# Performance work log

Hardware: AMD Instinct MI355X
Metric: run time of the kernel (lower is better)

## Reference

```python
import jax, jax.numpy as jnp
import numpy as np

B, T, D = 32, 4096, 256
LN_EPS = 1e-5


def setup_inputs() -> dict:
    key = jax.random.key(0)
    k0, k1, k2 = jax.random.split(key, 3)
    byte_ids = jax.random.randint(k0, (B, T), 0, 256, dtype=jnp.int32)
    freq_bands = jnp.ones((D // 2,), jnp.float32)  # nn.Parameter(torch.ones(embed_dim//2))
    # freq_proj: Linear(D, 2D) -> LayerNorm(2D) -> GELU -> Linear(2D, D)
    w1 = jax.random.normal(k1, (D, 2 * D), jnp.float32) * (1.0 / np.sqrt(D))
    b1 = jnp.zeros((2 * D,), jnp.float32)
    gamma = jnp.ones((2 * D,), jnp.float32)
    beta = jnp.zeros((2 * D,), jnp.float32)
    w2 = jax.random.normal(k2, (2 * D, D), jnp.float32) * (1.0 / np.sqrt(2 * D))
    b2 = jnp.zeros((D,), jnp.float32)
    return dict(byte_ids=byte_ids, freq_bands=freq_bands, w1=w1, b1=b1,
                gamma=gamma, beta=beta, w2=w2, b2=b2)


def reference(byte_ids, freq_bands, w1, b1, gamma, beta, w2, b2):
    Bsz, Tlen = byte_ids.shape
    Dm = w1.shape[0]
    k = min(Dm // 2, Tlen // 2)  # static
    signal = byte_ids.astype(jnp.float32) / 127.5 - 1.0  # [B,T]
    # Single FFT; FFT(roll(signal, -pos))[f] == X[f] * exp(+2i*pi*f*pos/T),
    # so |spectrum| is position-invariant and angle shifts linearly in pos.
    X = jnp.fft.fft(signal, axis=1)[:, :k]           # [B,k] complex64
    mag = jnp.abs(X) * freq_bands[:k]                 # [B,k]
    phase0 = jnp.angle(X)                             # [B,k]
    pos = jnp.arange(Tlen, dtype=jnp.float32)
    f = jnp.arange(k, dtype=jnp.float32)
    shift = (2.0 * np.pi / Tlen) * pos[:, None] * f[None, :]      # [T,k]
    phase = phase0[:, None, :] + shift[None, :, :]                 # [B,T,k]
    mag_bt = jnp.broadcast_to(mag[:, None, :], (Bsz, Tlen, k))     # [B,T,k]
    feats = jnp.concatenate([mag_bt, jnp.sin(phase), jnp.cos(phase)], axis=-1)  # [B,T,3k]
    if feats.shape[-1] < Dm:
        feats = jnp.pad(feats, ((0, 0), (0, 0), (0, Dm - feats.shape[-1])))
    else:
        feats = feats[..., :Dm]                        # truncate (drops cos tail)
    # freq_proj MLP
    h = feats @ w1 + b1                                # [B,T,2D]
    mu = jnp.mean(h, axis=-1, keepdims=True)
    var = jnp.var(h, axis=-1, keepdims=True)
    h = (h - mu) * jax.lax.rsqrt(var + LN_EPS) * gamma + beta
    h = jax.nn.gelu(h, approximate=False)              # torch nn.GELU default = exact erf
    return h @ w2 + b2                                 # [B,T,D]
```

## Files before the change

kernel.cpp:

```cpp
#include <hip/hip_runtime.h>


#define T_SZ   4096
#define NFREQ  128

typedef short    bf16x8 __attribute__((ext_vector_type(8)));
typedef unsigned u32x4  __attribute__((ext_vector_type(4)));
typedef float    f32x4  __attribute__((ext_vector_type(4)));

__device__ __forceinline__ float bf2f(unsigned short x) {
  union { unsigned u; float f; } v; v.u = ((unsigned)x) << 16; return v.f;
}
__device__ __forceinline__ float bits2f(unsigned u) {
  union { unsigned u; float f; } v; v.u = u; return v.f;
}
__device__ __forceinline__ unsigned short f2bf(float x) {
  union { float f; unsigned u; } v; v.f = x;
  unsigned r = v.u + 0x7fffu + ((v.u >> 16) & 1u);
  return (unsigned short)(r >> 16);
}
__device__ __forceinline__ unsigned pk2(float lo, float hi) {
  union { float f; unsigned u; } a, b;
  a.f = lo; b.f = hi;
  return __builtin_amdgcn_perm(b.u + 0x8000u, a.u + 0x8000u, 0x07060302u);
}
__device__ __forceinline__ bf16x8 as_bf(u32x4 v) { return __builtin_bit_cast(bf16x8, v); }
__device__ __forceinline__ bool probe_f32(const unsigned* p) {
  return p[0] == 0x3F800000u;
}
__device__ __forceinline__ void stage16(const void* g, const void* lds_base) {
  __builtin_amdgcn_global_load_lds(
      (const __attribute__((address_space(1))) unsigned int*)g,
      (__attribute__((address_space(3))) unsigned int*)lds_base, 16, 0, 0);
}
__device__ __forceinline__ float gelu_f(float v) {
  float u = v * (0.7978845608f + 0.0356774081f * v * v);
  float d = 1.0f + exp2f(-2.885390082f * u);
  return v * __builtin_amdgcn_rcpf(d);
}

__global__ void dft_kernel(const int* __restrict__ ids,
                           const void* __restrict__ fb,
                           unsigned short* __restrict__ mag,
                           float* __restrict__ ph0) {
  bool f32 = probe_f32((const unsigned*)fb);
  int b  = blockIdx.x >> 3;
  int fg = blockIdx.x & 7;
  int fl = threadIdx.x >> 4;
  int m  = threadIdx.x & 15;
  int f  = fg * 16 + fl;
  const int* row = ids + b * T_SZ;
  const float C = 6.283185307179586f / 4096.0f;
  float re = 0.f, im = 0.f;
  for (int i = 0; i < 256; ++i) {
    int t = m + i * 16;
    float s = (float)row[t] * (1.0f / 127.5f) - 1.0f;
    float ang = (float)((t * f) & 4095) * C;
    re += s * __cosf(ang);
    im -= s * __sinf(ang);
  }
  #pragma unroll
  for (int mask = 1; mask < 16; mask <<= 1) {
    re += __shfl_xor(re, mask, 64);
    im += __shfl_xor(im, mask, 64);
  }
  if (m == 0) {
    float fbv = f32 ? ((const float*)fb)[f] : bf2f(((const unsigned short*)fb)[f]);
    float mg = sqrtf(re * re + im * im) * fbv;
    mag[b * NFREQ + f] = f2bf(mg);
    ph0[b * NFREQ + f] = atan2f(im, re);
  }
}

__global__ void prep_kernel(const void* __restrict__ w1, const void* __restrict__ w2,
                            const void* __restrict__ b1, const void* __restrict__ gamma,
                            const void* __restrict__ beta, const void* __restrict__ b2,
                            const unsigned* __restrict__ probe,
                            const unsigned short* __restrict__ mag,
                            unsigned short* __restrict__ w1sin,
                            unsigned short* __restrict__ w2tp,
                            unsigned short* __restrict__ bia,
                            float* __restrict__ hmag) {
  bool f32 = probe_f32(probe);
  int bid = blockIdx.x, tid = threadIdx.x;
  if (bid < 256) {
    int o = bid * 256 + tid;
    int f = o & 127, n1 = o >> 7;
    int idx = (128 + f) * 512 + n1;
    w1sin[o] = f32 ? f2bf(((const float*)w1)[idx]) : ((const unsigned short*)w1)[idx];
  } else if (bid < 768) {
    int o = (bid - 256) * 256 + tid;
    int p = o & 511, n2 = o >> 9;
    int n1 = ((p >> 5) << 5) | (((p >> 2) & 1) << 4) | (((p >> 3) & 3) << 2) | (p & 3);
    int idx = n1 * 256 + n2;
    w2tp[o] = f32 ? f2bf(((const float*)w2)[idx]) : ((const unsigned short*)w2)[idx];
  } else if (bid < 832) {
    int idx = (bid - 768) * 256 + tid;
    int n1 = idx & 511, b = idx >> 9;
    const unsigned short* mrow = mag + b * NFREQ;
    float acc = 0.f;
    for (int f = 0; f < 128; ++f) {
      float wv = f32 ? ((const float*)w1)[f * 512 + n1]
                     : bf2f(((const unsigned short*)w1)[f * 512 + n1]);
      acc += bf2f(mrow[f]) * bf2f(f2bf(wv));
    }
    float bv = f32 ? ((const float*)b1)[n1] : bf2f(((const unsigned short*)b1)[n1]);
    hmag[idx] = acc + bv;
  } else {
    int i = (bid - 832) * 256 + tid;
    const void* src; int off;
    if (i < 512)       { src = gamma; off = i; }
    else if (i < 1024) { src = beta;  off = i - 512; }
    else               { src = b2;    off = i - 1024; }
    bia[i] = f32 ? f2bf(((const float*)src)[off]) : ((const unsigned short*)src)[off];
  }
}

__global__ __launch_bounds__(256, 2)
void fused_kernel(const unsigned short* __restrict__ w1sin,
                  const unsigned short* __restrict__ w2tp,
                  const unsigned short* __restrict__ bias,
                  const float* __restrict__ hmag,
                  const float* __restrict__ ph0,
                  float* __restrict__ out) {
  __shared__ __align__(16) short lds_w[16384];

  const int tid  = threadIdx.x;
  const int wave = tid >> 6;
  const int lane = tid & 63;
  const int quad = lane >> 4;
  const int col  = lane & 15;

  const int blk  = blockIdx.x;
  const int b    = blk >> 5;
  const int my_t = ((blk & 31) << 6) + (wave << 4) + col;

  {
    short* bufp = lds_w;
    #pragma unroll
    for (int i = 0; i < 4; ++i) {
      int rl = wave * 16 + i * 4 + quad;
      int gch = (lane & 15) ^ (rl & 15);
      stage16(w1sin + ((0 * 64 + rl) * 128 + gch * 8), bufp + (wave * 16 + i * 4) * 128);
    }
  }

  u32x4 BsA[4], BsB[4];
  const float* php = ph0 + b * NFREQ;
  const float PHC = 6.283185307179586f / 4096.0f;
  #pragma unroll
  for (int s = 0; s < 4; ++s) {
    u32x4 awA, awB;
    #pragma unroll
    for (int w = 0; w < 4; ++w) {
      int f0 = s * 32 + quad * 8 + w * 2;
      float a0 = __sinf(php[f0]     + (float)((my_t * f0) & 4095) * PHC);
      float a1 = __sinf(php[f0 + 1] + (float)((my_t * (f0 + 1)) & 4095) * PHC);
      awA[w] = pk2(a0, a1);
      awB[w] = awA[w] ^ 0x80000000u;
    }
    BsA[s] = awA; BsB[s] = awB;
  }

  __syncthreads();

  const float* hmagb = hmag + b * 512;
  u32x4 B2A[16], B2B[16];
  float sumA = 0.f, ssqA = 0.f, sumB = 0.f, ssqB = 0.f;
  #pragma unroll
  for (int h = 0; h < 8; ++h) {
    short* cur = lds_w + (h & 1) * 8192;
    short* nxt = lds_w + ((h + 1) & 1) * 8192;
    if (h < 7) {
      #pragma unroll
      for (int i = 0; i < 4; ++i) {
        int rl = wave * 16 + i * 4 + quad;
        int gch = (lane & 15) ^ (rl & 15);
        stage16(w1sin + (((h + 1) * 64 + rl) * 128 + gch * 8),
                nxt + (wave * 16 + i * 4) * 128);
      }
    } else {
      #pragma unroll
      for (int i = 0; i < 4; ++i) {
        int rl = i * 4 + wave;
        int gch = lane ^ (rl & 15);
        stage16(w2tp + ((0 * 16 + rl) * 512 + gch * 8), nxt + rl * 512);
      }
    }
    f32x4 pA = {0.f, 0.f, 0.f, 0.f}, pB = {0.f, 0.f, 0.f, 0.f};
    #pragma unroll
    for (int ntl = 0; ntl < 4; ++ntl) {
      f32x4 aA = *(const f32x4*)(hmagb + h * 64 + ntl * 16 + 4 * quad);
      f32x4 aB = aA;
      #pragma unroll
      for (int s = 0; s < 4; ++s) {
        bf16x8 frag = *(const bf16x8*)(cur + (ntl * 16 + col) * 128
                                           + (((s * 4 + quad) ^ col) << 3));
        aA = __builtin_amdgcn_mfma_f32_16x16x32_bf16(frag, as_bf(BsA[s]), aA, 0, 0, 0);
        aB = __builtin_amdgcn_mfma_f32_16x16x32_bf16(frag, as_bf(BsB[s]), aB, 0, 0, 0);
      }
      #pragma unroll
      for (int jj = 0; jj < 4; ++jj) {
        sumA += aA[jj]; ssqA += aA[jj] * aA[jj];
        sumB += aB[jj]; ssqB += aB[jj] * aB[jj];
      }
      if ((ntl & 1) == 0) { pA = aA; pB = aB; }
      else {
        int s2l = h * 2 + (ntl >> 1);
        u32x4 hA, hB;
        hA[0] = pk2(pA[0], pA[1]); hA[1] = pk2(pA[2], pA[3]);
        hA[2] = pk2(aA[0], aA[1]); hA[3] = pk2(aA[2], aA[3]);
        hB[0] = pk2(pB[0], pB[1]); hB[1] = pk2(pB[2], pB[3]);
        hB[2] = pk2(aB[0], aB[1]); hB[3] = pk2(aB[2], aB[3]);
        B2A[s2l] = hA;
        B2B[s2l] = hB;
      }
    }
    __syncthreads();
  }

  sumA += __shfl_xor(sumA, 16, 64); sumA += __shfl_xor(sumA, 32, 64);
  ssqA += __shfl_xor(ssqA, 16, 64); ssqA += __shfl_xor(ssqA, 32, 64);
  sumB += __shfl_xor(sumB, 16, 64); sumB += __shfl_xor(sumB, 32, 64);
  ssqB += __shfl_xor(ssqB, 16, 64); ssqB += __shfl_xor(ssqB, 32, 64);
  float muA = sumA * (1.0f / 512.0f);
  float varA = fmaxf(ssqA * (1.0f / 512.0f) - muA * muA, 0.0f);
  float rsA = rsqrtf(varA + 1e-5f);
  float muB = sumB * (1.0f / 512.0f);
  float varB = fmaxf(ssqB * (1.0f / 512.0f) - muB * muB, 0.0f);
  float rsB = rsqrtf(varB + 1e-5f);

  const unsigned short* gptr  = bias;
  const unsigned short* beptr = bias + 512;
  #pragma unroll
  for (int s2 = 0; s2 < 16; ++s2) {
    u32x4 hwA = B2A[s2], hwB = B2B[s2], owA, owB;
    #pragma unroll
    for (int w = 0; w < 4; ++w) {
      int nt  = 2 * s2 + (w >> 1);
      int n1b = nt * 16 + 4 * quad + (w & 1) * 2;
      unsigned gp = *(const unsigned*)(gptr + n1b);
      unsigned bp = *(const unsigned*)(beptr + n1b);
      float g0 = bits2f(gp << 16),  g1 = bits2f(gp & 0xffff0000u);
      float e0 = bits2f(bp << 16),  e1 = bits2f(bp & 0xffff0000u);
      float hA0 = bits2f(hwA[w] << 16), hA1 = bits2f(hwA[w] & 0xffff0000u);
      float hB0 = bits2f(hwB[w] << 16), hB1 = bits2f(hwB[w] & 0xffff0000u);
      float tA0 = rsA * g0, tA1 = rsA * g1;
      float tB0 = rsB * g0, tB1 = rsB * g1;
      float vA0 = fmaf(hA0, tA0, fmaf(-muA, tA0, e0));
      float vA1 = fmaf(hA1, tA1, fmaf(-muA, tA1, e1));
      float vB0 = fmaf(hB0, tB0, fmaf(-muB, tB0, e0));
      float vB1 = fmaf(hB1, tB1, fmaf(-muB, tB1, e1));
      owA[w] = pk2(gelu_f(vA0), gelu_f(vA1));
      owB[w] = pk2(gelu_f(vB0), gelu_f(vB1));
    }
    B2A[s2] = owA;
    B2B[s2] = owB;
  }

  const unsigned short* b2p = bias + 1024;
  const long orowA = (long)(b * T_SZ + my_t) * 256;
  const long orowB = orowA + (long)2048 * 256;
  #pragma unroll
  for (int h = 0; h < 16; ++h) {
    short* cur = lds_w + (h & 1) * 8192;
    short* nxt = lds_w + ((h + 1) & 1) * 8192;
    if (h < 15) {
      #pragma unroll
      for (int i = 0; i < 4; ++i) {
        int rl = i * 4 + wave;
        int gch = lane ^ (rl & 15);
        stage16(w2tp + (((h + 1) * 16 + rl) * 512 + gch * 8), nxt + rl * 512);
      }
    }
    f32x4 ccA = {0.f, 0.f, 0.f, 0.f};
    f32x4 ccB = {0.f, 0.f, 0.f, 0.f};
    #pragma unroll
    for (int s2 = 0; s2 < 16; ++s2) {
      bf16x8 A2 = *(const bf16x8*)(cur + col * 512 + (((s2 * 4 + quad) ^ col) << 3));
      ccA = __builtin_amdgcn_mfma_f32_16x16x32_bf16(A2, as_bf(B2A[s2]), ccA, 0, 0, 0);
      ccB = __builtin_amdgcn_mfma_f32_16x16x32_bf16(A2, as_bf(B2B[s2]), ccB, 0, 0, 0);
    }
    unsigned bp0 = *(const unsigned*)(b2p + h * 16 + 4 * quad);
    unsigned bp1 = *(const unsigned*)(b2p + h * 16 + 4 * quad + 2);
    float bb0 = bits2f(bp0 << 16), bb1 = bits2f(bp0 & 0xffff0000u);
    float bb2 = bits2f(bp1 << 16), bb3 = bits2f(bp1 & 0xffff0000u);
    ccA[0] += bb0; ccA[1] += bb1; ccA[2] += bb2; ccA[3] += bb3;
    ccB[0] += bb0; ccB[1] += bb1; ccB[2] += bb2; ccB[3] += bb3;
    *(f32x4*)(out + orowA + h * 16 + quad * 4) = ccA;
    *(f32x4*)(out + orowB + h * 16 + quad * 4) = ccB;
    if (h < 15) __syncthreads();
  }
}

extern "C" void kernel_launch(void* const* d_in, const int* in_sizes, int n_in,
                              void* d_out, int out_size, void* d_ws, size_t ws_size,
                              hipStream_t stream) {
  const int*      ids   = (const int*)d_in[0];
  const void*     fb    = d_in[1];
  const void*     w1    = d_in[2];
  const void*     b1    = d_in[3];
  const void*     gamma = d_in[4];
  const void*     beta  = d_in[5];
  const void*     w2    = d_in[6];
  const void*     b2    = d_in[7];
  float*          out   = (float*)d_out;
  const unsigned* probe = (const unsigned*)fb;

  char* ws = (char*)d_ws;
  unsigned short* mag   = (unsigned short*)(ws);
  float*          ph0   = (float*)(ws + 8192);
  unsigned short* bia   = (unsigned short*)(ws + 24576);
  float*          hmag  = (float*)(ws + 32768);
  unsigned short* w1sin = (unsigned short*)(ws + 98304);
  unsigned short* w2tp  = (unsigned short*)(ws + 229376);

  dft_kernel<<<dim3(32 * 8), dim3(256), 0, stream>>>(ids, fb, mag, ph0);
  prep_kernel<<<dim3(837), dim3(256), 0, stream>>>(w1, w2, b1, gamma, beta, b2,
                                                   probe, mag, w1sin, w2tp, bia, hmag);
  fused_kernel<<<dim3(1024), dim3(256), 0, stream>>>(w1sin, w2tp, bia, hmag, ph0, out);
}
```

Before: 258.9 us.

## Split DFT over time partitions, parallelize hmag reduction, dual-accumulate MFMA chain

The DFT now runs as 2048 blocks that each handle a 512-sample time slice and write partial sums, which a prep kernel then reduces. This raises parallelism above the old 256 serial-heavy blocks and vectorizes the id loads. The mag@w1 bias projection moves to its own kernel that splits the frequency sum across four waves and reduces through LDS. In the fused kernel, the second-GEMM MFMA chain uses two independent accumulators seeded with the bias, which shortens the dependency chain. The cost is an extra kernel launch and a workspace round trip for the partial sums.

```diff
diff --git a/kernel.cpp b/kernel.cpp
--- a/kernel.cpp
+++ b/kernel.cpp
@@ -39,80 +39,107 @@
   return v * __builtin_amdgcn_rcpf(d);
 }
 
-__global__ void dft_kernel(const int* __restrict__ ids,
-                           const void* __restrict__ fb,
-                           unsigned short* __restrict__ mag,
-                           float* __restrict__ ph0) {
-  bool f32 = probe_f32((const unsigned*)fb);
-  int b  = blockIdx.x >> 3;
-  int fg = blockIdx.x & 7;
+__global__ void dft_part_kernel(const int* __restrict__ ids,
+                                float2* __restrict__ part) {
+  int bid = blockIdx.x;
+  int b  = bid >> 6;
+  int fg = (bid >> 3) & 7;
+  int tp = bid & 7;
   int fl = threadIdx.x >> 4;
   int m  = threadIdx.x & 15;
   int f  = fg * 16 + fl;
-  const int* row = ids + b * T_SZ;
+  const int* row = ids + b * T_SZ + tp * 512;
   const float C = 6.283185307179586f / 4096.0f;
   float re = 0.f, im = 0.f;
-  for (int i = 0; i < 256; ++i) {
-    int t = m + i * 16;
-    float s = (float)row[t] * (1.0f / 127.5f) - 1.0f;
-    float ang = (float)((t * f) & 4095) * C;
-    re += s * __cosf(ang);
-    im -= s * __sinf(ang);
+  #pragma unroll
+  for (int i = 0; i < 8; ++i) {
+    int t0 = i * 64 + m * 4;
+    int4 iv = *(const int4*)(row + t0);
+    int a = ((tp * 512 + t0) * f) & 4095;
+#define DFT1(VAL) { float s = (float)(VAL) * (1.0f / 127.5f) - 1.0f;          \
+                    float ang = (float)a * C;                                 \
+                    re += s * __cosf(ang); im -= s * __sinf(ang);             \
+                    a = (a + f) & 4095; }
+    DFT1(iv.x) DFT1(iv.y) DFT1(iv.z) DFT1(iv.w)
+#undef DFT1
   }
   #pragma unroll
   for (int mask = 1; mask < 16; mask <<= 1) {
     re += __shfl_xor(re, mask, 64);
     im += __shfl_xor(im, mask, 64);
   }
-  if (m == 0) {
+  if (m == 0) part[(tp * 32 + b) * 128 + f] = make_float2(re, im);
+}
+
+__global__ void prep1_kernel(const void* __restrict__ w1, const void* __restrict__ w2,
+                             const void* __restrict__ gamma, const void* __restrict__ beta,
+                             const void* __restrict__ b2, const void* __restrict__ fb,
+                             const float2* __restrict__ part,
+                             unsigned short* __restrict__ mag,
+                             float* __restrict__ ph0,
+                             unsigned short* __restrict__ w1sin,
+                             unsigned short* __restrict__ w2tp,
+                             unsigned short* __restrict__ bia) {
+  bool f32 = probe_f32((const unsigned*)fb);
+  int bid = blockIdx.x, tid = threadIdx.x;
+  if (bid < 16) {
+    int idx = bid * 256 + tid;
+    int b = idx >> 7, f = idx & 127;
+    float re = 0.f, im = 0.f;
+    #pragma unroll
+    for (int p = 0; p < 8; ++p) {
+      float2 v = part[(p * 32 + b) * 128 + f];
+      re += v.x; im += v.y;
+    }
     float fbv = f32 ? ((const float*)fb)[f] : bf2f(((const unsigned short*)fb)[f]);
-    float mg = sqrtf(re * re + im * im) * fbv;
-    mag[b * NFREQ + f] = f2bf(mg);
+    mag[b * NFREQ + f] = f2bf(sqrtf(re * re + im * im) * fbv);
     ph0[b * NFREQ + f] = atan2f(im, re);
-  }
-}
-
-__global__ void prep_kernel(const void* __restrict__ w1, const void* __restrict__ w2,
-                            const void* __restrict__ b1, const void* __restrict__ gamma,
-                            const void* __restrict__ beta, const void* __restrict__ b2,
-                            const unsigned* __restrict__ probe,
-                            const unsigned short* __restrict__ mag,
-                            unsigned short* __restrict__ w1sin,
-                            unsigned short* __restrict__ w2tp,
-                            unsigned short* __restrict__ bia,
-                            float* __restrict__ hmag) {
-  bool f32 = probe_f32(probe);
-  int bid = blockIdx.x, tid = threadIdx.x;
-  if (bid < 256) {
-    int o = bid * 256 + tid;
+  } else if (bid < 272) {
+    int o = (bid - 16) * 256 + tid;
     int f = o & 127, n1 = o >> 7;
     int idx = (128 + f) * 512 + n1;
     w1sin[o] = f32 ? f2bf(((const float*)w1)[idx]) : ((const unsigned short*)w1)[idx];
-  } else if (bid < 768) {
-    int o = (bid - 256) * 256 + tid;
+  } else if (bid < 784) {
+    int o = (bid - 272) * 256 + tid;
     int p = o & 511, n2 = o >> 9;
     int n1 = ((p >> 5) << 5) | (((p >> 2) & 1) << 4) | (((p >> 3) & 3) << 2) | (p & 3);
     int idx = n1 * 256 + n2;
     w2tp[o] = f32 ? f2bf(((const float*)w2)[idx]) : ((const unsigned short*)w2)[idx];
-  } else if (bid < 832) {
-    int idx = (bid - 768) * 256 + tid;
-    int n1 = idx & 511, b = idx >> 9;
-    const unsigned short* mrow = mag + b * NFREQ;
-    float acc = 0.f;
-    for (int f = 0; f < 128; ++f) {
-      float wv = f32 ? ((const float*)w1)[f * 512 + n1]
-                     : bf2f(((const unsigned short*)w1)[f * 512 + n1]);
-      acc += bf2f(mrow[f]) * bf2f(f2bf(wv));
-    }
-    float bv = f32 ? ((const float*)b1)[n1] : bf2f(((const unsigned short*)b1)[n1]);
-    hmag[idx] = acc + bv;
   } else {
-    int i = (bid - 832) * 256 + tid;
+    int i = (bid - 784) * 256 + tid;
     const void* src; int off;
     if (i < 512)       { src = gamma; off = i; }
     else if (i < 1024) { src = beta;  off = i - 512; }
     else               { src = b2;    off = i - 1024; }
     bia[i] = f32 ? f2bf(((const float*)src)[off]) : ((const unsigned short*)src)[off];
+  }
+}
+
+__global__ void hmag_kernel(const void* __restrict__ w1, const void* __restrict__ b1,
+                            const unsigned* __restrict__ probe,
+                            const unsigned short* __restrict__ mag,
+                            float* __restrict__ hmag) {
+  __shared__ float red[256];
+  bool f32 = probe_f32(probe);
+  int bid = blockIdx.x;
+  int b = bid >> 3, n1g = bid & 7;
+  int tid = threadIdx.x;
+  int fq = tid >> 6, n1l = tid & 63;
+  int n1 = n1g * 64 + n1l;
+  const unsigned short* mrow = mag + b * NFREQ;
+  float acc = 0.f;
+  for (int f = fq * 32; f < fq * 32 + 32; ++f) {
+    float wv = f32 ? ((const float*)w1)[f * 512 + n1]
+                   : bf2f(((const unsigned short*)w1)[f * 512 + n1]);
+    acc += bf2f(mrow[f]) * bf2f(f2bf(wv));
+  }
+  red[tid] = acc;
+  __syncthreads();
+  if (tid < 64) {
+    int n1o = n1g * 64 + tid;
+    float a = red[tid] + red[64 + tid] + red[128 + tid] + red[192 + tid];
+    float bv = f32 ? ((const float*)b1)[n1o] : bf2f(((const unsigned short*)b1)[n1o]);
+    hmag[b * 512 + n1o] = a + bv;
   }
 }
 
@@ -273,20 +300,24 @@
         stage16(w2tp + (((h + 1) * 16 + rl) * 512 + gch * 8), nxt + rl * 512);
       }
     }
-    f32x4 ccA = {0.f, 0.f, 0.f, 0.f};
-    f32x4 ccB = {0.f, 0.f, 0.f, 0.f};
-    #pragma unroll
-    for (int s2 = 0; s2 < 16; ++s2) {
-      bf16x8 A2 = *(const bf16x8*)(cur + col * 512 + (((s2 * 4 + quad) ^ col) << 3));
-      ccA = __builtin_amdgcn_mfma_f32_16x16x32_bf16(A2, as_bf(B2A[s2]), ccA, 0, 0, 0);
-      ccB = __builtin_amdgcn_mfma_f32_16x16x32_bf16(A2, as_bf(B2B[s2]), ccB, 0, 0, 0);
-    }
     unsigned bp0 = *(const unsigned*)(b2p + h * 16 + 4 * quad);
     unsigned bp1 = *(const unsigned*)(b2p + h * 16 + 4 * quad + 2);
-    float bb0 = bits2f(bp0 << 16), bb1 = bits2f(bp0 & 0xffff0000u);
-    float bb2 = bits2f(bp1 << 16), bb3 = bits2f(bp1 & 0xffff0000u);
-    ccA[0] += bb0; ccA[1] += bb1; ccA[2] += bb2; ccA[3] += bb3;
-    ccB[0] += bb0; ccB[1] += bb1; ccB[2] += bb2; ccB[3] += bb3;
+    f32x4 ccA0 = { bits2f(bp0 << 16), bits2f(bp0 & 0xffff0000u),
+                   bits2f(bp1 << 16), bits2f(bp1 & 0xffff0000u) };
+    f32x4 ccB0 = ccA0;
+    f32x4 ccA1 = {0.f, 0.f, 0.f, 0.f};
+    f32x4 ccB1 = {0.f, 0.f, 0.f, 0.f};
+    #pragma unroll
+    for (int s2 = 0; s2 < 16; s2 += 2) {
+      bf16x8 A2a = *(const bf16x8*)(cur + col * 512 + (((s2 * 4 + quad) ^ col) << 3));
+      bf16x8 A2b = *(const bf16x8*)(cur + col * 512 + ((((s2 + 1) * 4 + quad) ^ col) << 3));
+      ccA0 = __builtin_amdgcn_mfma_f32_16x16x32_bf16(A2a, as_bf(B2A[s2]),     ccA0, 0, 0, 0);
+      ccB0 = __builtin_amdgcn_mfma_f32_16x16x32_bf16(A2a, as_bf(B2B[s2]),     ccB0, 0, 0, 0);
+      ccA1 = __builtin_amdgcn_mfma_f32_16x16x32_bf16(A2b, as_bf(B2A[s2 + 1]), ccA1, 0, 0, 0);
+      ccB1 = __builtin_amdgcn_mfma_f32_16x16x32_bf16(A2b, as_bf(B2B[s2 + 1]), ccB1, 0, 0, 0);
+    }
+    f32x4 ccA = ccA0 + ccA1;
+    f32x4 ccB = ccB0 + ccB1;
     *(f32x4*)(out + orowA + h * 16 + quad * 4) = ccA;
     *(f32x4*)(out + orowB + h * 16 + quad * 4) = ccB;
     if (h < 15) __syncthreads();
@@ -314,9 +345,11 @@
   float*          hmag  = (float*)(ws + 32768);
   unsigned short* w1sin = (unsigned short*)(ws + 98304);
   unsigned short* w2tp  = (unsigned short*)(ws + 229376);
-
-  dft_kernel<<<dim3(32 * 8), dim3(256), 0, stream>>>(ids, fb, mag, ph0);
-  prep_kernel<<<dim3(837), dim3(256), 0, stream>>>(w1, w2, b1, gamma, beta, b2,
-                                                   probe, mag, w1sin, w2tp, bia, hmag);
+  float2*         part  = (float2*)(ws + 491520);
+
+  dft_part_kernel<<<dim3(2048), dim3(256), 0, stream>>>(ids, part);
+  prep1_kernel<<<dim3(789), dim3(256), 0, stream>>>(w1, w2, gamma, beta, b2, fb,
+                                                    part, mag, ph0, w1sin, w2tp, bia);
+  hmag_kernel<<<dim3(256), dim3(256), 0, stream>>>(w1, b1, probe, mag, hmag);
   fused_kernel<<<dim3(1024), dim3(256), 0, stream>>>(w1sin, w2tp, bia, hmag, ph0, out);
 }
```

Result: faster. 244.1 us (-5.7%).
